# Optimization experiments

Measured on AMD Instinct MI355X. Metric: run time of the kernel, lower is better.

The kernel has to match this reference:

```python
import jax, jax.numpy as jnp
import numpy as np

NUM_NODES = 512

def chebyshev_convolution(laplacian, signal, weights, t0):
    # Faithful port of the torch helper, including tk_prev staying equal to
    # `laplacian` throughout the loop (as in the source).
    k = weights.shape[0]
    # t0 is the identity, so t0 @ signal == signal
    out = jnp.matmul(signal, weights[0])
    out = out + jnp.matmul(jnp.matmul(laplacian, signal), weights[1])
    tk_prev = laplacian
    tk = 2.0 * jnp.matmul(laplacian, laplacian) - t0
    for i in range(2, k):
        out = out + jnp.matmul(jnp.matmul(tk, signal), weights[i])
        tk = 2.0 * jnp.matmul(laplacian, tk) - tk_prev
    return out


def setup_inputs() -> dict:
    key = jax.random.key(0)
    ks = jax.random.split(key, 5)
    B, T, N, C_IN, C_OUT, CS, CD = 4, 12, NUM_NODES, 64, 64, 3, 6
    std_l = 0.1 / np.sqrt(N)
    std_t = 0.1 / np.sqrt(C_IN)
    x = jax.random.normal(ks[0], (B, T, N, C_IN), dtype=jnp.float32)
    ws = jax.random.uniform(ks[1], (N, N), jnp.float32, -std_l, std_l)
    ts = jax.random.uniform(ks[2], (CS, C_IN, C_OUT), jnp.float32, -std_t, std_t)
    wp = jax.random.uniform(ks[3], (C_IN, C_IN), jnp.float32, -std_t, std_t)
    td = jax.random.uniform(ks[4], (CD, C_IN, C_OUT), jnp.float32, -std_t, std_t)
    return {"x": x, "ws": ws, "ts": ts, "wp": wp, "td": td}


def reference(x, ws, ts, wp, td):
    N = NUM_NODES
    t0 = jnp.eye(N, dtype=x.dtype)
    # Static (SGC) branch: Chebyshev conv with learned static Laplacian ws
    out_s = chebyshev_convolution(ws, x, ts, t0)
    # Dynamic branch: data-dependent Laplacian wd = x @ (wp @ x^T)  -> (B,T,N,N)
    wd = jnp.matmul(x, jnp.matmul(wp, jnp.swapaxes(x, -2, -1)))
    wd = wd + jnp.min(wd)
    wd = wd / jnp.max(wd) / (N ** 2)
    out_d = chebyshev_convolution(wd, x, td, t0)
    return out_s + out_d
```

## Files before the change

kernel.cpp:

```cpp
#include <hip/hip_runtime.h>
#include <cstddef>
#include <cstdint>

#define NN 512
#define CC 64
#define BT 48

typedef __bf16 bf16_t;
typedef bf16_t bf16x8 __attribute__((ext_vector_type(8)));
typedef bf16_t bf16x4 __attribute__((ext_vector_type(4)));
typedef float f32x4 __attribute__((ext_vector_type(4)));

#define OFF_MN    0
#define OFF_MX    384
#define OFF_WSB   1024
#define OFF_WS2B  132096
#define OFF_XBT   263168
#define OFF_XNB   1049600
#define OFF_XNR   1836032
#define OFF_CS0   2622464
#define OFF_WEB   2647040
#define OFF_WER   2745344
#define OFF_VDY   2843648
#define OFF_T1T   2846720
#define OFF_T2T   2848768

__device__ __forceinline__ f32x4 mfma(bf16x8 a, bf16x8 b, f32x4 c) {
  return __builtin_amdgcn_mfma_f32_16x16x32_bf16(a, b, c, 0, 0, 0);
}
__device__ __forceinline__ int swz_chunk(int r, int c8) {
  return r * 64 + ((c8 ^ (r & 7)) << 3);
}
__device__ __forceinline__ int swz_e(int r, int c) {
  return r * 64 + ((((c >> 3) ^ (r & 7)) << 3)) + (c & 7);
}
__device__ __forceinline__ bf16x8 frag(const bf16_t* sm, int row, int kc) {
  return *(const bf16x8*)(sm + row * 64 + ((kc ^ (row & 7)) << 3));
}
__device__ __forceinline__ void stage64(bf16_t* sm, const bf16_t* g, int ld, int tid) {
#pragma unroll
  for (int j = 0; j < 2; ++j) {
    int id = tid + 256 * j;
    int r = id >> 3, c8 = id & 7;
    bf16x8 v = *(const bf16x8*)(g + (size_t)r * ld + c8 * 8);
    *(bf16x8*)(sm + swz_chunk(r, c8)) = v;
  }
}
__device__ __forceinline__ void stage64f(bf16_t* sm, const float* g, int ld, int tid) {
#pragma unroll
  for (int j = 0; j < 4; ++j) {
    int idx = tid + 256 * j;
    int r = idx >> 4, cc = (idx & 15) * 4;
    float4 v = *(const float4*)(g + (size_t)r * ld + cc);
    bf16x4 o = {(bf16_t)v.x, (bf16_t)v.y, (bf16_t)v.z, (bf16_t)v.w};
    *(bf16x4*)(sm + swz_e(r, cc)) = o;
  }
}
struct bfpair { bf16_t b, r; };
__device__ __forceinline__ bfpair splitbf(float f) {
  bfpair p;
  p.b = (bf16_t)f;
  p.r = (bf16_t)(f - (float)p.b);
  return p;
}

__global__ __launch_bounds__(256) void k_preA(
    const float* __restrict__ x, const float* __restrict__ wp,
    float* __restrict__ wsf)
{
  __shared__ __align__(16) char pool[32768];
  __shared__ float red[16];
  const int tid = threadIdx.x;
  const int b = blockIdx.x;
  const int w = tid >> 6, l = tid & 63, lh = l >> 4, lr = l & 15, m0 = w * 16;

  if (b < 384) {
    const int bt = (b & 7) + 8 * (b >> 6);
    const int it = (b >> 3) & 7;
    const int i0 = it * 64;
    float (*XsF)[66] = (float(*)[66])pool;
    bf16_t* XBT = (bf16_t*)(wsf + OFF_XBT);
    bf16_t* XNb = (bf16_t*)(wsf + OFF_XNB);
    bf16_t* XNr = (bf16_t*)(wsf + OFF_XNR);
    float* CS0 = wsf + OFF_CS0;
    const float* xg = x + ((size_t)bt * NN + i0) * CC;
    for (int j = 0; j < 4; ++j) {
      int idx = tid + 256 * j;
      int r = idx >> 4, c0v = (idx & 15) * 4;
      float4 v = *(const float4*)(xg + (size_t)r * CC + c0v);
      bfpair p0 = splitbf(v.x), p1 = splitbf(v.y), p2 = splitbf(v.z), p3 = splitbf(v.w);
      bf16x4 vb = {p0.b, p1.b, p2.b, p3.b};
      bf16x4 vr = {p0.r, p1.r, p2.r, p3.r};
      size_t gb = ((size_t)bt * 512 + i0 + r) * 64 + c0v;
      *(bf16x4*)(XNb + gb) = vb;
      *(bf16x4*)(XNr + gb) = vr;
      XsF[c0v + 0][r] = v.x; XsF[c0v + 1][r] = v.y;
      XsF[c0v + 2][r] = v.z; XsF[c0v + 3][r] = v.w;
    }
    __syncthreads();
    {
      int c = tid >> 2, k0 = (tid & 3) * 16;
      bf16x8 o1, o2;
#pragma unroll
      for (int q = 0; q < 8; ++q) {
        o1[q] = (bf16_t)XsF[c][k0 + q];
        o2[q] = (bf16_t)XsF[c][k0 + 8 + q];
      }
      size_t base = ((size_t)bt * 64 + c) * 512 + i0 + k0;
      *(bf16x8*)(XBT + base) = o1; *(bf16x8*)(XBT + base + 8) = o2;
    }
    if (tid < 64) {
      float s = 0.f;
      for (int r = 0; r < 64; ++r) s += XsF[tid][r];
      CS0[((size_t)bt * 8 + it) * 64 + tid] = s;
    }
    return;
  }
  const int g = b - 384;
  const int bt = (g & 7) + 8 * (g >> 6);
  const int bx = (g >> 3) & 7;
  bf16_t* WpT  = (bf16_t*)pool;
  bf16_t* Xa   = (bf16_t*)(pool + 8192);
  bf16_t* Hs   = (bf16_t*)(pool + 16384);
  bf16_t* Xcol = (bf16_t*)(pool + 24576);
  for (int j = 0; j < 4; ++j) {
    int idx = tid + 256 * j;
    int r = idx >> 4, cc = (idx & 15) * 4;
    float4 v = *(const float4*)(wp + r * 64 + cc);
    WpT[swz_e(cc + 0, r)] = (bf16_t)v.x;
    WpT[swz_e(cc + 1, r)] = (bf16_t)v.y;
    WpT[swz_e(cc + 2, r)] = (bf16_t)v.z;
    WpT[swz_e(cc + 3, r)] = (bf16_t)v.w;
  }
  stage64f(Xa, x + ((size_t)bt * NN + bx * 64) * CC, 64, tid);
  __syncthreads();
  f32x4 hacc[4] = {};
#pragma unroll
  for (int q = 0; q < 2; ++q) {
    bf16x8 a = frag(Xa, m0 + lr, q * 4 + lh);
#pragma unroll
    for (int t = 0; t < 4; ++t)
      hacc[t] = mfma(a, frag(WpT, t * 16 + lr, q * 4 + lh), hacc[t]);
  }
#pragma unroll
  for (int t = 0; t < 4; ++t)
#pragma unroll
    for (int r_ = 0; r_ < 4; ++r_)
      Hs[swz_e(m0 + 4 * lh + r_, t * 16 + lr)] = (bf16_t)hacc[t][r_];
  float mn = 3.4e38f, mx = -3.4e38f;
  for (int byj = 0; byj < 8; ++byj) {
    __syncthreads();
    stage64f(Xcol, x + ((size_t)bt * NN + byj * 64) * CC, 64, tid);
    __syncthreads();
    f32x4 acc[4] = {};
#pragma unroll
    for (int q = 0; q < 2; ++q) {
      bf16x8 a = frag(Hs, m0 + lr, q * 4 + lh);
#pragma unroll
      for (int t = 0; t < 4; ++t)
        acc[t] = mfma(a, frag(Xcol, t * 16 + lr, q * 4 + lh), acc[t]);
    }
#pragma unroll
    for (int t = 0; t < 4; ++t)
#pragma unroll
      for (int r_ = 0; r_ < 4; ++r_) {
        mn = fminf(mn, acc[t][r_]); mx = fmaxf(mx, acc[t][r_]);
      }
  }
  for (int off = 32; off; off >>= 1) {
    mn = fminf(mn, __shfl_xor(mn, off));
    mx = fmaxf(mx, __shfl_xor(mx, off));
  }
  if (l == 0) { red[w] = mn; red[8 + w] = mx; }
  __syncthreads();
  if (tid == 0) {
    mn = fminf(fminf(red[0], red[1]), fminf(red[2], red[3]));
    mx = fmaxf(fmaxf(red[8], red[9]), fmaxf(red[10], red[11]));
    wsf[OFF_MN + g] = mn; wsf[OFF_MX + g] = mx;
  }
}

__global__ __launch_bounds__(256) void k_mid(
    const float* __restrict__ wsL, const float* __restrict__ ts,
    const float* __restrict__ wp, const float* __restrict__ td,
    float* __restrict__ wsf)
{
  __shared__ __align__(16) char pool[91712];
  const int tid = threadIdx.x;
  const int b = blockIdx.x;
  const int w = tid >> 6, l = tid & 63, lh = l >> 4, lr = l & 15, m0 = w * 16;

  if (b >= 48) {
    if (b < 112) {
      const int idx2 = b - 48;
      bf16_t* Asb = (bf16_t*)pool;
      bf16_t* Bsb = (bf16_t*)(pool + 8192);
      bf16_t* Ys  = (bf16_t*)(pool + 16384);
      bf16_t* WS2B = (bf16_t*)(wsf + OFF_WS2B);
      const int r0 = (idx2 >> 3) * 64, c0 = (idx2 & 7) * 64;
      f32x4 acc[4] = {};
      for (int jj = 0; jj < 8; ++jj) {
        if (jj) __syncthreads();
        for (int j = 0; j < 4; ++j) {
          int idx = tid + 256 * j;
          int r = idx >> 4, cc = (idx & 15) * 4;
          float4 v = *(const float4*)(wsL + (size_t)(r0 + r) * 512 + jj * 64 + cc);
          bf16x4 vb = {(bf16_t)v.x, (bf16_t)v.y, (bf16_t)v.z, (bf16_t)v.w};
          *(bf16x4*)(Asb + swz_e(r, cc)) = vb;
          float4 u = *(const float4*)(wsL + (size_t)(jj * 64 + r) * 512 + c0 + cc);
          Bsb[swz_e(cc + 0, r)] = (bf16_t)u.x;
          Bsb[swz_e(cc + 1, r)] = (bf16_t)u.y;
          Bsb[swz_e(cc + 2, r)] = (bf16_t)u.z;
          Bsb[swz_e(cc + 3, r)] = (bf16_t)u.w;
        }
        __syncthreads();
#pragma unroll
        for (int q = 0; q < 2; ++q) {
          bf16x8 a = frag(Asb, m0 + lr, q * 4 + lh);
#pragma unroll
          for (int t = 0; t < 4; ++t)
            acc[t] = mfma(a, frag(Bsb, t * 16 + lr, q * 4 + lh), acc[t]);
        }
      }
#pragma unroll
      for (int t = 0; t < 4; ++t)
#pragma unroll
        for (int r_ = 0; r_ < 4; ++r_) {
          int row = m0 + 4 * lh + r_, col = t * 16 + lr;
          float v = 2.0f * acc[t][r_] - ((r0 + row) == (c0 + col) ? 1.0f : 0.0f);
          Ys[swz_e(row, col)] = (bf16_t)v;
        }
      __syncthreads();
#pragma unroll
      for (int j = 0; j < 2; ++j) {
        int id = tid + 256 * j;
        int r = id >> 3, c8 = id & 7;
        *(bf16x8*)(WS2B + (size_t)(r0 + r) * 512 + c0 + c8 * 8) =
            *(const bf16x8*)(Ys + swz_chunk(r, c8));
      }
      return;
    }
    if (b < 120) {
      const int bx = b - 112;
      const float* wrow = wsL + (size_t)bx * 64 * 512;
      bf16_t* wob = (bf16_t*)(wsf + OFF_WSB) + (size_t)bx * 64 * 512;
      for (int j = 0; j < 32; ++j) {
        int idx = tid + 256 * j;
        float4 v = *(const float4*)(wrow + (size_t)idx * 4);
        bf16x4 o = {(bf16_t)v.x, (bf16_t)v.y, (bf16_t)v.z, (bf16_t)v.w};
        *(bf16x4*)(wob + (size_t)idx * 4) = o;
      }
      return;
    }
    {
      bf16_t* T1 = (bf16_t*)(wsf + OFF_T1T);
      bf16_t* T2 = (bf16_t*)(wsf + OFF_T2T);
      const float* t1g = ts + 4096;
      const float* t2g = ts + 8192;
      for (int j = 0; j < 16; ++j) {
        int idx = tid + 256 * j;
        int cin = idx >> 6, co = idx & 63;
        T1[co * 64 + cin] = (bf16_t)t1g[cin * 64 + co];
        T2[co * 64 + cin] = (bf16_t)t2g[cin * 64 + co];
      }
      return;
    }
  }
  const int bt = b;
  bf16_t* XB  = (bf16_t*)pool;
  bf16_t* Ab0 = (bf16_t*)pool;
  bf16_t* AT0 = (bf16_t*)(pool + 8192);
  bf16_t* Ab1 = (bf16_t*)(pool + 16384);
  bf16_t* AT1 = (bf16_t*)(pool + 24576);
  bf16_t* Gb  = (bf16_t*)(pool + 32768);
  bf16_t* WpT = (bf16_t*)(pool + 40960);
  bf16_t* WpN = (bf16_t*)(pool + 49152);
  bf16_t* tdA = (bf16_t*)(pool + 57344);
  bf16_t* tdB = (bf16_t*)(pool + 65536);
  float (*P0F)[66] = (float(*)[66])(pool + 73728);
  float* vec = (float*)(pool + 90624);
  float* uF = vec;        float* hF = vec + 64;
  float* b0 = vec + 128;  float* b1 = vec + 192;
  float* redv = vec + 256;
  const bf16_t* XBTg = (const bf16_t*)(wsf + OFF_XBT);
  const float* CS0 = wsf + OFF_CS0;
  for (int kk = 0; kk < 8; ++kk)
    stage64(XB + kk * 4096, XBTg + (size_t)bt * 32768 + kk * 64, 512, tid);
  {
    float mn = 3.4e38f, mx = -3.4e38f;
    for (int i = tid; i < 384; i += 256) {
      mn = fminf(mn, wsf[OFF_MN + i]);
      mx = fmaxf(mx, wsf[OFF_MX + i]);
    }
    for (int off = 32; off; off >>= 1) {
      mn = fminf(mn, __shfl_xor(mn, off));
      mx = fmaxf(mx, __shfl_xor(mx, off));
    }
    if (l == 0) { redv[w] = mn; redv[8 + w] = mx; }
  }
  if (tid < 64) {
    float s = 0.f;
#pragma unroll
    for (int p = 0; p < 8; ++p) s += CS0[((size_t)bt * 8 + p) * 64 + tid];
    uF[tid] = s;
  }
  __syncthreads();
  f32x4 pacc[4] = {};
  for (int kk = 0; kk < 8; ++kk) {
    const bf16_t* xt = XB + kk * 4096;
#pragma unroll
    for (int q = 0; q < 2; ++q) {
      bf16x8 a = frag(xt, m0 + lr, q * 4 + lh);
#pragma unroll
      for (int t = 0; t < 4; ++t)
        pacc[t] = mfma(a, frag(xt, t * 16 + lr, q * 4 + lh), pacc[t]);
    }
  }
  const float mnA = fminf(fminf(redv[0], redv[1]), fminf(redv[2], redv[3]));
  const float mxA = fmaxf(fmaxf(redv[8], redv[9]), fmaxf(redv[10], redv[11]));
  const float s_sc = 1.0f / (mxA + mnA) / 262144.0f;
  const float c_sc = mnA * s_sc;
  __syncthreads();
#pragma unroll
  for (int t = 0; t < 4; ++t)
#pragma unroll
    for (int r_ = 0; r_ < 4; ++r_) {
      int m = m0 + 4 * lh + r_, jc = t * 16 + lr;
      float pv = pacc[t][r_];
      P0F[m][jc] = pv;
      bf16_t bv = (bf16_t)pv;
      Ab0[swz_e(m, jc)] = bv; AT0[swz_e(jc, m)] = bv;
    }
  for (int j = 0; j < 4; ++j) {
    int idx = tid + 256 * j;
    int r = idx >> 4, cc = (idx & 15) * 4;
    float4 v = *(const float4*)(wp + r * 64 + cc);
    bf16_t q0 = (bf16_t)v.x, q1 = (bf16_t)v.y, q2 = (bf16_t)v.z, q3 = (bf16_t)v.w;
    WpN[swz_e(r, cc + 0)] = q0; WpT[swz_e(cc + 0, r)] = q0;
    WpN[swz_e(r, cc + 1)] = q1; WpT[swz_e(cc + 1, r)] = q1;
    WpN[swz_e(r, cc + 2)] = q2; WpT[swz_e(cc + 2, r)] = q2;
    WpN[swz_e(r, cc + 3)] = q3; WpT[swz_e(cc + 3, r)] = q3;
  }
  for (int j = 0; j < 4; ++j) {
    int idx = tid + 256 * j;
    int cin = idx >> 4, co = (idx & 15) * 4;
    float4 v = *(const float4*)(td + 4096 + cin * 64 + co);
    tdA[swz_e(co + 0, cin)] = (bf16_t)v.x;
    tdA[swz_e(co + 1, cin)] = (bf16_t)v.y;
    tdA[swz_e(co + 2, cin)] = (bf16_t)v.z;
    tdA[swz_e(co + 3, cin)] = (bf16_t)v.w;
  }
  if (tid < 64) b0[tid] = uF[tid];
  __syncthreads();
  {
    int jj = tid >> 2, sub = tid & 3;
    float s = 0.f;
    for (int c = sub * 16; c < sub * 16 + 16; ++c)
      s += (float)WpT[swz_e(jj, c)] * uF[c];
    s += __shfl_xor(s, 1); s += __shfl_xor(s, 2);
    if (sub == 0) hF[jj] = s;
  }
  {
    f32x4 g[4] = {};
#pragma unroll
    for (int q = 0; q < 2; ++q) {
      bf16x8 a = frag(Ab0, m0 + lr, q * 4 + lh);
#pragma unroll
      for (int t = 0; t < 4; ++t)
        g[t] = mfma(a, frag(WpT, t * 16 + lr, q * 4 + lh), g[t]);
    }
#pragma unroll
    for (int t = 0; t < 4; ++t)
#pragma unroll
      for (int r_ = 0; r_ < 4; ++r_)
        Gb[swz_e(m0 + 4 * lh + r_, t * 16 + lr)] = (bf16_t)g[t][r_];
  }
  __syncthreads();
  float mu = 0.f, vacc = 0.f;
  f32x4 Macc[4] = {};
  for (int i = 1; i <= 5; ++i) {
    const float* bcur = (i & 1) ? b0 : b1;
    float* bnx = (i & 1) ? b1 : b0;
    const bf16_t* tdc = (i & 1) ? tdA : tdB;
    const bf16_t* AbC = (i & 1) ? Ab0 : Ab1;
    const bf16_t* ATC = (i & 1) ? AT0 : AT1;
    bf16_t* AbN = (i & 1) ? Ab1 : Ab0;
    bf16_t* ATN = (i & 1) ? AT1 : AT0;
    if (i < 5) {
      bf16_t* tdn = (i & 1) ? tdB : tdA;
      for (int j = 0; j < 4; ++j) {
        int idx = tid + 256 * j;
        int cin = idx >> 4, co = (idx & 15) * 4;
        float4 v = *(const float4*)(td + (i + 1) * 4096 + cin * 64 + co);
        tdn[swz_e(co + 0, cin)] = (bf16_t)v.x;
        tdn[swz_e(co + 1, cin)] = (bf16_t)v.y;
        tdn[swz_e(co + 2, cin)] = (bf16_t)v.z;
        tdn[swz_e(co + 3, cin)] = (bf16_t)v.w;
      }
    }
#pragma unroll
    for (int q = 0; q < 2; ++q) {
      bf16x8 a = frag(AbC, m0 + lr, q * 4 + lh);
#pragma unroll
      for (int t = 0; t < 4; ++t)
        Macc[t] = mfma(a, frag(tdc, t * 16 + lr, q * 4 + lh), Macc[t]);
    }
    f32x4 Aacc[4] = {};
    if (i < 5) {
#pragma unroll
      for (int q = 0; q < 2; ++q) {
        bf16x8 g = frag(Gb, m0 + lr, q * 4 + lh);
#pragma unroll
        for (int t = 0; t < 4; ++t)
          Aacc[t] = mfma(g, frag(ATC, t * 16 + lr, q * 4 + lh), Aacc[t]);
      }
    }
    {
      int co = tid >> 2, sub = tid & 3;
      float sv = 0.f;
      for (int c = sub * 16; c < sub * 16 + 16; ++c)
        sv += bcur[c] * (float)tdc[swz_e(co, c)];
      sv += __shfl_xor(sv, 1); sv += __shfl_xor(sv, 2);
      if (sub == 0) vacc += sv;
    }
    if (i < 5) {
      int jj = tid >> 2, sub = tid & 3;
      float t1 = 0.f;
      for (int m = sub * 16; m < sub * 16 + 16; ++m)
        t1 += (float)ATC[swz_e(jj, m)] * hF[m];
      t1 += __shfl_xor(t1, 1); t1 += __shfl_xor(t1, 2);
      if (sub == 0)
        bnx[jj] = 2.f * (s_sc * t1 + 512.f * c_sc * bcur[jj] + mu * uF[jj])
                  - (i >= 2 ? uF[jj] : 0.f);
    }
    if (i < 5) {
#pragma unroll
      for (int t = 0; t < 4; ++t)
#pragma unroll
        for (int r_ = 0; r_ < 4; ++r_) {
          int m = m0 + 4 * lh + r_, jc = t * 16 + lr;
          float v = 2.f * (s_sc * Aacc[t][r_] + c_sc * uF[m] * bcur[jc] + mu * P0F[m][jc])
                    - (i >= 2 ? P0F[m][jc] : 0.f);
          bf16_t bv = (bf16_t)v;
          AbN[swz_e(m, jc)] = bv; ATN[swz_e(jc, m)] = bv;
        }
      mu = (i == 1) ? -1.f : 0.f;
    }
    __syncthreads();
  }
  bf16_t* Mst = tdA;
#pragma unroll
  for (int t = 0; t < 4; ++t)
#pragma unroll
    for (int r_ = 0; r_ < 4; ++r_)
      Mst[swz_e(t * 16 + lr, m0 + 4 * lh + r_)] = (bf16_t)Macc[t][r_];
  __syncthreads();
  f32x4 wm[4] = {};
#pragma unroll
  for (int q = 0; q < 2; ++q) {
    bf16x8 a = frag(WpN, m0 + lr, q * 4 + lh);
#pragma unroll
    for (int t = 0; t < 4; ++t)
      wm[t] = mfma(a, frag(Mst, t * 16 + lr, q * 4 + lh), wm[t]);
  }
  bf16_t* WEb = (bf16_t*)(wsf + OFF_WEB);
  bf16_t* WEr = (bf16_t*)(wsf + OFF_WER);
#pragma unroll
  for (int t = 0; t < 4; ++t)
#pragma unroll
    for (int r_ = 0; r_ < 4; ++r_) {
      int a_ = m0 + 4 * lh + r_, co = t * 16 + lr;
      float weff = ts[a_ * 64 + co] + td[a_ * 64 + co] - td[2 * 4096 + a_ * 64 + co]
                   + s_sc * wm[t][r_];
      bfpair p = splitbf(weff);
      WEb[((size_t)bt * 64 + co) * 64 + a_] = p.b;
      WEr[((size_t)bt * 64 + co) * 64 + a_] = p.r;
    }
  if ((tid & 3) == 0) (wsf + OFF_VDY)[bt * 64 + (tid >> 2)] = c_sc * vacc;
}

__global__ __launch_bounds__(256) void k_out(float* __restrict__ wsf,
                                             float* __restrict__ out)
{
  __shared__ __align__(16) char pool[73728];
  bf16_t* As  = (bf16_t*)pool;
  bf16_t* B1  = (bf16_t*)(pool + 8192);
  bf16_t* B2  = (bf16_t*)(pool + 16384);
  bf16_t* Z1s = As;
  bf16_t* Z2s = B1;
  bf16_t* Xb  = (bf16_t*)(pool + 24576);
  bf16_t* Xr  = (bf16_t*)(pool + 32768);
  bf16_t* WEs = (bf16_t*)(pool + 40960);
  bf16_t* WRs = (bf16_t*)(pool + 49152);
  bf16_t* T1s = (bf16_t*)(pool + 57344);
  bf16_t* T2s = (bf16_t*)(pool + 65536);
  const int tid = threadIdx.x;
  const int g = blockIdx.x;
  const int bt = (g & 7) + 8 * (g >> 6);
  const int n0 = ((g >> 3) & 7) * 64;
  const int w = tid >> 6, l = tid & 63, lh = l >> 4, lr = l & 15, m0 = w * 16;
  stage64(Xb,  (const bf16_t*)(wsf + OFF_XNB) + ((size_t)bt * 512 + n0) * 64, 64, tid);
  stage64(Xr,  (const bf16_t*)(wsf + OFF_XNR) + ((size_t)bt * 512 + n0) * 64, 64, tid);
  stage64(WEs, (const bf16_t*)(wsf + OFF_WEB) + (size_t)bt * 4096, 64, tid);
  stage64(WRs, (const bf16_t*)(wsf + OFF_WER) + (size_t)bt * 4096, 64, tid);
  stage64(T1s, (const bf16_t*)(wsf + OFF_T1T), 64, tid);
  stage64(T2s, (const bf16_t*)(wsf + OFF_T2T), 64, tid);
  const bf16_t* XBT = (const bf16_t*)(wsf + OFF_XBT);
  const bf16_t* WSB = (const bf16_t*)(wsf + OFF_WSB);
  const bf16_t* WS2B = (const bf16_t*)(wsf + OFF_WS2B);
  f32x4 acc1[4] = {}, acc2[4] = {};
  for (int kk = 0; kk < 8; ++kk) {
    if (kk) __syncthreads();
    stage64(As, XBT + (size_t)bt * 32768 + kk * 64, 512, tid);
    stage64(B1, WSB + (size_t)n0 * 512 + kk * 64, 512, tid);
    stage64(B2, WS2B + (size_t)n0 * 512 + kk * 64, 512, tid);
    __syncthreads();
#pragma unroll
    for (int q = 0; q < 2; ++q) {
      bf16x8 a = frag(As, m0 + lr, q * 4 + lh);
#pragma unroll
      for (int t = 0; t < 4; ++t) {
        acc1[t] = mfma(a, frag(B1, t * 16 + lr, q * 4 + lh), acc1[t]);
        acc2[t] = mfma(a, frag(B2, t * 16 + lr, q * 4 + lh), acc2[t]);
      }
    }
  }
  __syncthreads();
#pragma unroll
  for (int t = 0; t < 4; ++t)
#pragma unroll
    for (int r_ = 0; r_ < 4; ++r_) {
      int cy = m0 + 4 * lh + r_, nl = t * 16 + lr;
      Z1s[swz_e(nl, cy)] = (bf16_t)acc1[t][r_];
      Z2s[swz_e(nl, cy)] = (bf16_t)acc2[t][r_];
    }
  __syncthreads();
  const float* VDY = wsf + OFF_VDY;
  f32x4 accO[4];
#pragma unroll
  for (int t = 0; t < 4; ++t) {
    float vv = VDY[bt * 64 + t * 16 + lr];
    accO[t] = {vv, vv, vv, vv};
  }
#pragma unroll
  for (int q = 0; q < 2; ++q) {
    bf16x8 aXb = frag(Xb, m0 + lr, q * 4 + lh);
    bf16x8 aXr = frag(Xr, m0 + lr, q * 4 + lh);
    bf16x8 aZ1 = frag(Z1s, m0 + lr, q * 4 + lh);
    bf16x8 aZ2 = frag(Z2s, m0 + lr, q * 4 + lh);
#pragma unroll
    for (int t = 0; t < 4; ++t) {
      bf16x8 bWb = frag(WEs, t * 16 + lr, q * 4 + lh);
      bf16x8 bWr = frag(WRs, t * 16 + lr, q * 4 + lh);
      accO[t] = mfma(aXb, bWb, accO[t]);
      accO[t] = mfma(aXb, bWr, accO[t]);
      accO[t] = mfma(aXr, bWb, accO[t]);
      accO[t] = mfma(aZ1, frag(T1s, t * 16 + lr, q * 4 + lh), accO[t]);
      accO[t] = mfma(aZ2, frag(T2s, t * 16 + lr, q * 4 + lh), accO[t]);
    }
  }
#pragma unroll
  for (int t = 0; t < 4; ++t)
#pragma unroll
    for (int r_ = 0; r_ < 4; ++r_)
      out[((size_t)bt * 512 + n0 + m0 + 4 * lh + r_) * 64 + t * 16 + lr] = accO[t][r_];
}

extern "C" void kernel_launch(void* const* d_in, const int* in_sizes, int n_in,
                              void* d_out, int out_size, void* d_ws, size_t ws_size,
                              hipStream_t stream)
{
  (void)in_sizes; (void)n_in; (void)out_size; (void)ws_size;
  const float* x   = (const float*)d_in[0];
  const float* wsL = (const float*)d_in[1];
  const float* ts  = (const float*)d_in[2];
  const float* wp  = (const float*)d_in[3];
  const float* td  = (const float*)d_in[4];
  float* out = (float*)d_out;
  float* wsf = (float*)d_ws;
  dim3 b(256);

  k_preA<<<768, b, 0, stream>>>(x, wp, wsf);
  k_mid <<<121, b, 0, stream>>>(wsL, ts, wp, td, wsf);
  k_out <<<384, b, 0, stream>>>(wsf, out);
}
```

Before: 44.66 us.

## Fuse per-batch weight derivation into output kernel, dropping the middle launch

The three-kernel pipeline becomes two. The static-Laplacian squaring, bf16 casting and transposes move into the prologue kernel. The per-bt Chebyshev recurrence that builds the effective weights now runs inside each output block, reusing the X^T X product it computes alongside the Z GEMMs. This removes a launch and the global round trip for WEb/WEr/VDY. In exchange, each bt's recurrence is repeated in 8 blocks, and the larger LDS footprint may lower occupancy.

```diff
diff --git a/kernel.cpp b/kernel.cpp
--- a/kernel.cpp
+++ b/kernel.cpp
@@ -19,11 +19,8 @@
 #define OFF_XNB   1049600
 #define OFF_XNR   1836032
 #define OFF_CS0   2622464
-#define OFF_WEB   2647040
-#define OFF_WER   2745344
-#define OFF_VDY   2843648
-#define OFF_T1T   2846720
-#define OFF_T2T   2848768
+#define OFF_T1T   2647040
+#define OFF_T2T   2649088
 
 __device__ __forceinline__ f32x4 mfma(bf16x8 a, bf16x8 b, f32x4 c) {
   return __builtin_amdgcn_mfma_f32_16x16x32_bf16(a, b, c, 0, 0, 0);
@@ -64,8 +61,9 @@
   return p;
 }
 
-__global__ __launch_bounds__(256) void k_preA(
-    const float* __restrict__ x, const float* __restrict__ wp,
+__global__ __launch_bounds__(256) void k_pre(
+    const float* __restrict__ x, const float* __restrict__ wsL,
+    const float* __restrict__ ts, const float* __restrict__ wp,
     float* __restrict__ wsf)
 {
   __shared__ __align__(16) char pool[32768];
@@ -116,158 +114,186 @@
     }
     return;
   }
-  const int g = b - 384;
+  if (b < 768) {
+    const int g = b - 384;
+    const int bt = (g & 7) + 8 * (g >> 6);
+    const int bx = (g >> 3) & 7;
+    bf16_t* WpT  = (bf16_t*)pool;
+    bf16_t* Xa   = (bf16_t*)(pool + 8192);
+    bf16_t* Hs   = (bf16_t*)(pool + 16384);
+    bf16_t* Xcol = (bf16_t*)(pool + 24576);
+    for (int j = 0; j < 4; ++j) {
+      int idx = tid + 256 * j;
+      int r = idx >> 4, cc = (idx & 15) * 4;
+      float4 v = *(const float4*)(wp + r * 64 + cc);
+      WpT[swz_e(cc + 0, r)] = (bf16_t)v.x;
+      WpT[swz_e(cc + 1, r)] = (bf16_t)v.y;
+      WpT[swz_e(cc + 2, r)] = (bf16_t)v.z;
+      WpT[swz_e(cc + 3, r)] = (bf16_t)v.w;
+    }
+    stage64f(Xa, x + ((size_t)bt * NN + bx * 64) * CC, 64, tid);
+    __syncthreads();
+    f32x4 hacc[4] = {};
+#pragma unroll
+    for (int q = 0; q < 2; ++q) {
+      bf16x8 a = frag(Xa, m0 + lr, q * 4 + lh);
+#pragma unroll
+      for (int t = 0; t < 4; ++t)
+        hacc[t] = mfma(a, frag(WpT, t * 16 + lr, q * 4 + lh), hacc[t]);
+    }
+#pragma unroll
+    for (int t = 0; t < 4; ++t)
+#pragma unroll
+      for (int r_ = 0; r_ < 4; ++r_)
+        Hs[swz_e(m0 + 4 * lh + r_, t * 16 + lr)] = (bf16_t)hacc[t][r_];
+    float mn = 3.4e38f, mx = -3.4e38f;
+    for (int byj = 0; byj < 8; ++byj) {
+      __syncthreads();
+      stage64f(Xcol, x + ((size_t)bt * NN + byj * 64) * CC, 64, tid);
+      __syncthreads();
+      f32x4 acc[4] = {};
+#pragma unroll
+      for (int q = 0; q < 2; ++q) {
+        bf16x8 a = frag(Hs, m0 + lr, q * 4 + lh);
+#pragma unroll
+        for (int t = 0; t < 4; ++t)
+          acc[t] = mfma(a, frag(Xcol, t * 16 + lr, q * 4 + lh), acc[t]);
+      }
+#pragma unroll
+      for (int t = 0; t < 4; ++t)
+#pragma unroll
+        for (int r_ = 0; r_ < 4; ++r_) {
+          mn = fminf(mn, acc[t][r_]); mx = fmaxf(mx, acc[t][r_]);
+        }
+    }
+    for (int off = 32; off; off >>= 1) {
+      mn = fminf(mn, __shfl_xor(mn, off));
+      mx = fmaxf(mx, __shfl_xor(mx, off));
+    }
+    if (l == 0) { red[w] = mn; red[8 + w] = mx; }
+    __syncthreads();
+    if (tid == 0) {
+      mn = fminf(fminf(red[0], red[1]), fminf(red[2], red[3]));
+      mx = fmaxf(fmaxf(red[8], red[9]), fmaxf(red[10], red[11]));
+      wsf[OFF_MN + g] = mn; wsf[OFF_MX + g] = mx;
+    }
+    return;
+  }
+  if (b < 832) {
+    const int idx2 = b - 768;
+    bf16_t* Asb = (bf16_t*)pool;
+    bf16_t* Bsb = (bf16_t*)(pool + 8192);
+    bf16_t* Ys  = (bf16_t*)(pool + 16384);
+    bf16_t* WS2B = (bf16_t*)(wsf + OFF_WS2B);
+    const int r0 = (idx2 >> 3) * 64, c0 = (idx2 & 7) * 64;
+    f32x4 acc[4] = {};
+    for (int jj = 0; jj < 8; ++jj) {
+      if (jj) __syncthreads();
+      for (int j = 0; j < 4; ++j) {
+        int idx = tid + 256 * j;
+        int r = idx >> 4, cc = (idx & 15) * 4;
+        float4 v = *(const float4*)(wsL + (size_t)(r0 + r) * 512 + jj * 64 + cc);
+        bf16x4 vb = {(bf16_t)v.x, (bf16_t)v.y, (bf16_t)v.z, (bf16_t)v.w};
+        *(bf16x4*)(Asb + swz_e(r, cc)) = vb;
+        float4 u = *(const float4*)(wsL + (size_t)(jj * 64 + r) * 512 + c0 + cc);
+        Bsb[swz_e(cc + 0, r)] = (bf16_t)u.x;
+        Bsb[swz_e(cc + 1, r)] = (bf16_t)u.y;
+        Bsb[swz_e(cc + 2, r)] = (bf16_t)u.z;
+        Bsb[swz_e(cc + 3, r)] = (bf16_t)u.w;
+      }
+      __syncthreads();
+#pragma unroll
+      for (int q = 0; q < 2; ++q) {
+        bf16x8 a = frag(Asb, m0 + lr, q * 4 + lh);
+#pragma unroll
+        for (int t = 0; t < 4; ++t)
+          acc[t] = mfma(a, frag(Bsb, t * 16 + lr, q * 4 + lh), acc[t]);
+      }
+    }
+#pragma unroll
+    for (int t = 0; t < 4; ++t)
+#pragma unroll
+      for (int r_ = 0; r_ < 4; ++r_) {
+        int row = m0 + 4 * lh + r_, col = t * 16 + lr;
+        float v = 2.0f * acc[t][r_] - ((r0 + row) == (c0 + col) ? 1.0f : 0.0f);
+        Ys[swz_e(row, col)] = (bf16_t)v;
+      }
+    __syncthreads();
+#pragma unroll
+    for (int j = 0; j < 2; ++j) {
+      int id = tid + 256 * j;
+      int r = id >> 3, c8 = id & 7;
+      *(bf16x8*)(WS2B + (size_t)(r0 + r) * 512 + c0 + c8 * 8) =
+          *(const bf16x8*)(Ys + swz_chunk(r, c8));
+    }
+    return;
+  }
+  if (b < 840) {
+    const int bx = b - 832;
+    const float* wrow = wsL + (size_t)bx * 64 * 512;
+    bf16_t* wob = (bf16_t*)(wsf + OFF_WSB) + (size_t)bx * 64 * 512;
+    for (int j = 0; j < 32; ++j) {
+      int idx = tid + 256 * j;
+      float4 v = *(const float4*)(wrow + (size_t)idx * 4);
+      bf16x4 o = {(bf16_t)v.x, (bf16_t)v.y, (bf16_t)v.z, (bf16_t)v.w};
+      *(bf16x4*)(wob + (size_t)idx * 4) = o;
+    }
+    return;
+  }
+  {
+    bf16_t* T1 = (bf16_t*)(wsf + OFF_T1T);
+    bf16_t* T2 = (bf16_t*)(wsf + OFF_T2T);
+    const float* t1g = ts + 4096;
+    const float* t2g = ts + 8192;
+    for (int j = 0; j < 16; ++j) {
+      int idx = tid + 256 * j;
+      int cin = idx >> 6, co = idx & 63;
+      T1[co * 64 + cin] = (bf16_t)t1g[cin * 64 + co];
+      T2[co * 64 + cin] = (bf16_t)t2g[cin * 64 + co];
+    }
+  }
+}
+
+__global__ __launch_bounds__(256) void k_go(
+    const float* __restrict__ ts, const float* __restrict__ wp,
+    const float* __restrict__ td, float* __restrict__ wsf,
+    float* __restrict__ out)
+{
+  __shared__ __align__(16) char pool[81920];
+  const int tid = threadIdx.x;
+  const int g = blockIdx.x;
   const int bt = (g & 7) + 8 * (g >> 6);
-  const int bx = (g >> 3) & 7;
-  bf16_t* WpT  = (bf16_t*)pool;
-  bf16_t* Xa   = (bf16_t*)(pool + 8192);
-  bf16_t* Hs   = (bf16_t*)(pool + 16384);
-  bf16_t* Xcol = (bf16_t*)(pool + 24576);
-  for (int j = 0; j < 4; ++j) {
-    int idx = tid + 256 * j;
-    int r = idx >> 4, cc = (idx & 15) * 4;
-    float4 v = *(const float4*)(wp + r * 64 + cc);
-    WpT[swz_e(cc + 0, r)] = (bf16_t)v.x;
-    WpT[swz_e(cc + 1, r)] = (bf16_t)v.y;
-    WpT[swz_e(cc + 2, r)] = (bf16_t)v.z;
-    WpT[swz_e(cc + 3, r)] = (bf16_t)v.w;
-  }
-  stage64f(Xa, x + ((size_t)bt * NN + bx * 64) * CC, 64, tid);
+  const int n0 = ((g >> 3) & 7) * 64;
+  const int w = tid >> 6, l = tid & 63, lh = l >> 4, lr = l & 15, m0 = w * 16;
+
+  bf16_t* XB = (bf16_t*)pool;
+  bf16_t* B1 = (bf16_t*)(pool + 65536);
+  bf16_t* B2 = (bf16_t*)(pool + 73728);
+  const bf16_t* XBTg = (const bf16_t*)(wsf + OFF_XBT);
+  const bf16_t* WSB  = (const bf16_t*)(wsf + OFF_WSB);
+  const bf16_t* WS2B = (const bf16_t*)(wsf + OFF_WS2B);
+  for (int kk = 0; kk < 8; ++kk)
+    stage64(XB + kk * 4096, XBTg + (size_t)bt * 32768 + kk * 64, 512, tid);
+  f32x4 acc1[4] = {}, acc2[4] = {}, pacc[4] = {};
+  for (int kk = 0; kk < 8; ++kk) {
+    __syncthreads();
+    stage64(B1, WSB + (size_t)n0 * 512 + kk * 64, 512, tid);
+    stage64(B2, WS2B + (size_t)n0 * 512 + kk * 64, 512, tid);
+    __syncthreads();
+    const bf16_t* xt = XB + kk * 4096;
+#pragma unroll
+    for (int q = 0; q < 2; ++q) {
+      bf16x8 a = frag(xt, m0 + lr, q * 4 + lh);
+#pragma unroll
+      for (int t = 0; t < 4; ++t) {
+        acc1[t] = mfma(a, frag(B1, t * 16 + lr, q * 4 + lh), acc1[t]);
+        acc2[t] = mfma(a, frag(B2, t * 16 + lr, q * 4 + lh), acc2[t]);
+        pacc[t] = mfma(a, frag(xt, t * 16 + lr, q * 4 + lh), pacc[t]);
+      }
+    }
+  }
   __syncthreads();
-  f32x4 hacc[4] = {};
-#pragma unroll
-  for (int q = 0; q < 2; ++q) {
-    bf16x8 a = frag(Xa, m0 + lr, q * 4 + lh);
-#pragma unroll
-    for (int t = 0; t < 4; ++t)
-      hacc[t] = mfma(a, frag(WpT, t * 16 + lr, q * 4 + lh), hacc[t]);
-  }
-#pragma unroll
-  for (int t = 0; t < 4; ++t)
-#pragma unroll
-    for (int r_ = 0; r_ < 4; ++r_)
-      Hs[swz_e(m0 + 4 * lh + r_, t * 16 + lr)] = (bf16_t)hacc[t][r_];
-  float mn = 3.4e38f, mx = -3.4e38f;
-  for (int byj = 0; byj < 8; ++byj) {
-    __syncthreads();
-    stage64f(Xcol, x + ((size_t)bt * NN + byj * 64) * CC, 64, tid);
-    __syncthreads();
-    f32x4 acc[4] = {};
-#pragma unroll
-    for (int q = 0; q < 2; ++q) {
-      bf16x8 a = frag(Hs, m0 + lr, q * 4 + lh);
-#pragma unroll
-      for (int t = 0; t < 4; ++t)
-        acc[t] = mfma(a, frag(Xcol, t * 16 + lr, q * 4 + lh), acc[t]);
-    }
-#pragma unroll
-    for (int t = 0; t < 4; ++t)
-#pragma unroll
-      for (int r_ = 0; r_ < 4; ++r_) {
-        mn = fminf(mn, acc[t][r_]); mx = fmaxf(mx, acc[t][r_]);
-      }
-  }
-  for (int off = 32; off; off >>= 1) {
-    mn = fminf(mn, __shfl_xor(mn, off));
-    mx = fmaxf(mx, __shfl_xor(mx, off));
-  }
-  if (l == 0) { red[w] = mn; red[8 + w] = mx; }
-  __syncthreads();
-  if (tid == 0) {
-    mn = fminf(fminf(red[0], red[1]), fminf(red[2], red[3]));
-    mx = fmaxf(fmaxf(red[8], red[9]), fmaxf(red[10], red[11]));
-    wsf[OFF_MN + g] = mn; wsf[OFF_MX + g] = mx;
-  }
-}
-
-__global__ __launch_bounds__(256) void k_mid(
-    const float* __restrict__ wsL, const float* __restrict__ ts,
-    const float* __restrict__ wp, const float* __restrict__ td,
-    float* __restrict__ wsf)
-{
-  __shared__ __align__(16) char pool[91712];
-  const int tid = threadIdx.x;
-  const int b = blockIdx.x;
-  const int w = tid >> 6, l = tid & 63, lh = l >> 4, lr = l & 15, m0 = w * 16;
-
-  if (b >= 48) {
-    if (b < 112) {
-      const int idx2 = b - 48;
-      bf16_t* Asb = (bf16_t*)pool;
-      bf16_t* Bsb = (bf16_t*)(pool + 8192);
-      bf16_t* Ys  = (bf16_t*)(pool + 16384);
-      bf16_t* WS2B = (bf16_t*)(wsf + OFF_WS2B);
-      const int r0 = (idx2 >> 3) * 64, c0 = (idx2 & 7) * 64;
-      f32x4 acc[4] = {};
-      for (int jj = 0; jj < 8; ++jj) {
-        if (jj) __syncthreads();
-        for (int j = 0; j < 4; ++j) {
-          int idx = tid + 256 * j;
-          int r = idx >> 4, cc = (idx & 15) * 4;
-          float4 v = *(const float4*)(wsL + (size_t)(r0 + r) * 512 + jj * 64 + cc);
-          bf16x4 vb = {(bf16_t)v.x, (bf16_t)v.y, (bf16_t)v.z, (bf16_t)v.w};
-          *(bf16x4*)(Asb + swz_e(r, cc)) = vb;
-          float4 u = *(const float4*)(wsL + (size_t)(jj * 64 + r) * 512 + c0 + cc);
-          Bsb[swz_e(cc + 0, r)] = (bf16_t)u.x;
-          Bsb[swz_e(cc + 1, r)] = (bf16_t)u.y;
-          Bsb[swz_e(cc + 2, r)] = (bf16_t)u.z;
-          Bsb[swz_e(cc + 3, r)] = (bf16_t)u.w;
-        }
-        __syncthreads();
-#pragma unroll
-        for (int q = 0; q < 2; ++q) {
-          bf16x8 a = frag(Asb, m0 + lr, q * 4 + lh);
-#pragma unroll
-          for (int t = 0; t < 4; ++t)
-            acc[t] = mfma(a, frag(Bsb, t * 16 + lr, q * 4 + lh), acc[t]);
-        }
-      }
-#pragma unroll
-      for (int t = 0; t < 4; ++t)
-#pragma unroll
-        for (int r_ = 0; r_ < 4; ++r_) {
-          int row = m0 + 4 * lh + r_, col = t * 16 + lr;
-          float v = 2.0f * acc[t][r_] - ((r0 + row) == (c0 + col) ? 1.0f : 0.0f);
-          Ys[swz_e(row, col)] = (bf16_t)v;
-        }
-      __syncthreads();
-#pragma unroll
-      for (int j = 0; j < 2; ++j) {
-        int id = tid + 256 * j;
-        int r = id >> 3, c8 = id & 7;
-        *(bf16x8*)(WS2B + (size_t)(r0 + r) * 512 + c0 + c8 * 8) =
-            *(const bf16x8*)(Ys + swz_chunk(r, c8));
-      }
-      return;
-    }
-    if (b < 120) {
-      const int bx = b - 112;
-      const float* wrow = wsL + (size_t)bx * 64 * 512;
-      bf16_t* wob = (bf16_t*)(wsf + OFF_WSB) + (size_t)bx * 64 * 512;
-      for (int j = 0; j < 32; ++j) {
-        int idx = tid + 256 * j;
-        float4 v = *(const float4*)(wrow + (size_t)idx * 4);
-        bf16x4 o = {(bf16_t)v.x, (bf16_t)v.y, (bf16_t)v.z, (bf16_t)v.w};
-        *(bf16x4*)(wob + (size_t)idx * 4) = o;
-      }
-      return;
-    }
-    {
-      bf16_t* T1 = (bf16_t*)(wsf + OFF_T1T);
-      bf16_t* T2 = (bf16_t*)(wsf + OFF_T2T);
-      const float* t1g = ts + 4096;
-      const float* t2g = ts + 8192;
-      for (int j = 0; j < 16; ++j) {
-        int idx = tid + 256 * j;
-        int cin = idx >> 6, co = idx & 63;
-        T1[co * 64 + cin] = (bf16_t)t1g[cin * 64 + co];
-        T2[co * 64 + cin] = (bf16_t)t2g[cin * 64 + co];
-      }
-      return;
-    }
-  }
-  const int bt = b;
-  bf16_t* XB  = (bf16_t*)pool;
+
   bf16_t* Ab0 = (bf16_t*)pool;
   bf16_t* AT0 = (bf16_t*)(pool + 8192);
   bf16_t* Ab1 = (bf16_t*)(pool + 16384);
@@ -277,15 +303,12 @@
   bf16_t* WpN = (bf16_t*)(pool + 49152);
   bf16_t* tdA = (bf16_t*)(pool + 57344);
   bf16_t* tdB = (bf16_t*)(pool + 65536);
-  float (*P0F)[66] = (float(*)[66])(pool + 73728);
-  float* vec = (float*)(pool + 90624);
-  float* uF = vec;        float* hF = vec + 64;
-  float* b0 = vec + 128;  float* b1 = vec + 192;
-  float* redv = vec + 256;
-  const bf16_t* XBTg = (const bf16_t*)(wsf + OFF_XBT);
+  float* vec = (float*)(pool + 73728);
+  float* uF = vec;         float* hF = vec + 64;
+  float* b0 = vec + 128;   float* b1 = vec + 192;
+  float* vaccF = vec + 256;
+  float* redv = vec + 320;
   const float* CS0 = wsf + OFF_CS0;
-  for (int kk = 0; kk < 8; ++kk)
-    stage64(XB + kk * 4096, XBTg + (size_t)bt * 32768 + kk * 64, 512, tid);
   {
     float mn = 3.4e38f, mx = -3.4e38f;
     for (int i = tid; i < 384; i += 256) {
@@ -298,39 +321,20 @@
     }
     if (l == 0) { redv[w] = mn; redv[8 + w] = mx; }
   }
+#pragma unroll
+  for (int t = 0; t < 4; ++t)
+#pragma unroll
+    for (int r_ = 0; r_ < 4; ++r_) {
+      int m = m0 + 4 * lh + r_, jc = t * 16 + lr;
+      bf16_t bv = (bf16_t)pacc[t][r_];
+      Ab0[swz_e(m, jc)] = bv; AT0[swz_e(jc, m)] = bv;
+    }
   if (tid < 64) {
     float s = 0.f;
 #pragma unroll
     for (int p = 0; p < 8; ++p) s += CS0[((size_t)bt * 8 + p) * 64 + tid];
-    uF[tid] = s;
-  }
-  __syncthreads();
-  f32x4 pacc[4] = {};
-  for (int kk = 0; kk < 8; ++kk) {
-    const bf16_t* xt = XB + kk * 4096;
-#pragma unroll
-    for (int q = 0; q < 2; ++q) {
-      bf16x8 a = frag(xt, m0 + lr, q * 4 + lh);
-#pragma unroll
-      for (int t = 0; t < 4; ++t)
-        pacc[t] = mfma(a, frag(xt, t * 16 + lr, q * 4 + lh), pacc[t]);
-    }
-  }
-  const float mnA = fminf(fminf(redv[0], redv[1]), fminf(redv[2], redv[3]));
-  const float mxA = fmaxf(fmaxf(redv[8], redv[9]), fmaxf(redv[10], redv[11]));
-  const float s_sc = 1.0f / (mxA + mnA) / 262144.0f;
-  const float c_sc = mnA * s_sc;
-  __syncthreads();
-#pragma unroll
-  for (int t = 0; t < 4; ++t)
-#pragma unroll
-    for (int r_ = 0; r_ < 4; ++r_) {
-      int m = m0 + 4 * lh + r_, jc = t * 16 + lr;
-      float pv = pacc[t][r_];
-      P0F[m][jc] = pv;
-      bf16_t bv = (bf16_t)pv;
-      Ab0[swz_e(m, jc)] = bv; AT0[swz_e(jc, m)] = bv;
-    }
+    uF[tid] = s; b0[tid] = s; vaccF[tid] = 0.f;
+  }
   for (int j = 0; j < 4; ++j) {
     int idx = tid + 256 * j;
     int r = idx >> 4, cc = (idx & 15) * 4;
@@ -350,8 +354,11 @@
     tdA[swz_e(co + 2, cin)] = (bf16_t)v.z;
     tdA[swz_e(co + 3, cin)] = (bf16_t)v.w;
   }
-  if (tid < 64) b0[tid] = uF[tid];
   __syncthreads();
+  const float mnA = fminf(fminf(redv[0], redv[1]), fminf(redv[2], redv[3]));
+  const float mxA = fmaxf(fmaxf(redv[8], redv[9]), fmaxf(redv[10], redv[11]));
+  const float s_sc = 1.0f / (mxA + mnA) / 262144.0f;
+  const float c_sc = mnA * s_sc;
   {
     int jj = tid >> 2, sub = tid & 3;
     float s = 0.f;
@@ -361,22 +368,22 @@
     if (sub == 0) hF[jj] = s;
   }
   {
-    f32x4 g[4] = {};
+    f32x4 gv[4] = {};
 #pragma unroll
     for (int q = 0; q < 2; ++q) {
       bf16x8 a = frag(Ab0, m0 + lr, q * 4 + lh);
 #pragma unroll
       for (int t = 0; t < 4; ++t)
-        g[t] = mfma(a, frag(WpT, t * 16 + lr, q * 4 + lh), g[t]);
+        gv[t] = mfma(a, frag(WpT, t * 16 + lr, q * 4 + lh), gv[t]);
     }
 #pragma unroll
     for (int t = 0; t < 4; ++t)
 #pragma unroll
       for (int r_ = 0; r_ < 4; ++r_)
-        Gb[swz_e(m0 + 4 * lh + r_, t * 16 + lr)] = (bf16_t)g[t][r_];
+        Gb[swz_e(m0 + 4 * lh + r_, t * 16 + lr)] = (bf16_t)gv[t][r_];
   }
   __syncthreads();
-  float mu = 0.f, vacc = 0.f;
+  float mu = 0.f;
   f32x4 Macc[4] = {};
   for (int i = 1; i <= 5; ++i) {
     const float* bcur = (i & 1) ? b0 : b1;
@@ -409,10 +416,10 @@
     if (i < 5) {
 #pragma unroll
       for (int q = 0; q < 2; ++q) {
-        bf16x8 g = frag(Gb, m0 + lr, q * 4 + lh);
+        bf16x8 gfr = frag(Gb, m0 + lr, q * 4 + lh);
 #pragma unroll
         for (int t = 0; t < 4; ++t)
-          Aacc[t] = mfma(g, frag(ATC, t * 16 + lr, q * 4 + lh), Aacc[t]);
+          Aacc[t] = mfma(gfr, frag(ATC, t * 16 + lr, q * 4 + lh), Aacc[t]);
       }
     }
     {
@@ -421,7 +428,7 @@
       for (int c = sub * 16; c < sub * 16 + 16; ++c)
         sv += bcur[c] * (float)tdc[swz_e(co, c)];
       sv += __shfl_xor(sv, 1); sv += __shfl_xor(sv, 2);
-      if (sub == 0) vacc += sv;
+      if (sub == 0) vaccF[co] += sv;
     }
     if (i < 5) {
       int jj = tid >> 2, sub = tid & 3;
@@ -439,8 +446,8 @@
 #pragma unroll
         for (int r_ = 0; r_ < 4; ++r_) {
           int m = m0 + 4 * lh + r_, jc = t * 16 + lr;
-          float v = 2.f * (s_sc * Aacc[t][r_] + c_sc * uF[m] * bcur[jc] + mu * P0F[m][jc])
-                    - (i >= 2 ? P0F[m][jc] : 0.f);
+          float v = 2.f * (s_sc * Aacc[t][r_] + c_sc * uF[m] * bcur[jc] + mu * pacc[t][r_])
+                    - (i >= 2 ? pacc[t][r_] : 0.f);
           bf16_t bv = (bf16_t)v;
           AbN[swz_e(m, jc)] = bv; ATN[swz_e(jc, m)] = bv;
         }
@@ -463,8 +470,16 @@
     for (int t = 0; t < 4; ++t)
       wm[t] = mfma(a, frag(Mst, t * 16 + lr, q * 4 + lh), wm[t]);
   }
-  bf16_t* WEb = (bf16_t*)(wsf + OFF_WEB);
-  bf16_t* WEr = (bf16_t*)(wsf + OFF_WER);
+  __syncthreads();
+
+  bf16_t* Z1s = (bf16_t*)pool;
+  bf16_t* Z2s = (bf16_t*)(pool + 8192);
+  bf16_t* Xb  = (bf16_t*)(pool + 16384);
+  bf16_t* Xr  = (bf16_t*)(pool + 24576);
+  bf16_t* WEs = (bf16_t*)(pool + 32768);
+  bf16_t* WRs = (bf16_t*)(pool + 40960);
+  bf16_t* T1s = (bf16_t*)(pool + 49152);
+  bf16_t* T2s = (bf16_t*)(pool + 57344);
 #pragma unroll
   for (int t = 0; t < 4; ++t)
 #pragma unroll
@@ -473,73 +488,21 @@
       float weff = ts[a_ * 64 + co] + td[a_ * 64 + co] - td[2 * 4096 + a_ * 64 + co]
                    + s_sc * wm[t][r_];
       bfpair p = splitbf(weff);
-      WEb[((size_t)bt * 64 + co) * 64 + a_] = p.b;
-      WEr[((size_t)bt * 64 + co) * 64 + a_] = p.r;
-    }
-  if ((tid & 3) == 0) (wsf + OFF_VDY)[bt * 64 + (tid >> 2)] = c_sc * vacc;
-}
-
-__global__ __launch_bounds__(256) void k_out(float* __restrict__ wsf,
-                                             float* __restrict__ out)
-{
-  __shared__ __align__(16) char pool[73728];
-  bf16_t* As  = (bf16_t*)pool;
-  bf16_t* B1  = (bf16_t*)(pool + 8192);
-  bf16_t* B2  = (bf16_t*)(pool + 16384);
-  bf16_t* Z1s = As;
-  bf16_t* Z2s = B1;
-  bf16_t* Xb  = (bf16_t*)(pool + 24576);
-  bf16_t* Xr  = (bf16_t*)(pool + 32768);
-  bf16_t* WEs = (bf16_t*)(pool + 40960);
-  bf16_t* WRs = (bf16_t*)(pool + 49152);
-  bf16_t* T1s = (bf16_t*)(pool + 57344);
-  bf16_t* T2s = (bf16_t*)(pool + 65536);
-  const int tid = threadIdx.x;
-  const int g = blockIdx.x;
-  const int bt = (g & 7) + 8 * (g >> 6);
-  const int n0 = ((g >> 3) & 7) * 64;
-  const int w = tid >> 6, l = tid & 63, lh = l >> 4, lr = l & 15, m0 = w * 16;
+      WEs[swz_e(co, a_)] = p.b;
+      WRs[swz_e(co, a_)] = p.r;
+      int cy = a_, nl = co;
+      Z1s[swz_e(nl, cy)] = (bf16_t)acc1[t][r_];
+      Z2s[swz_e(nl, cy)] = (bf16_t)acc2[t][r_];
+    }
   stage64(Xb,  (const bf16_t*)(wsf + OFF_XNB) + ((size_t)bt * 512 + n0) * 64, 64, tid);
   stage64(Xr,  (const bf16_t*)(wsf + OFF_XNR) + ((size_t)bt * 512 + n0) * 64, 64, tid);
-  stage64(WEs, (const bf16_t*)(wsf + OFF_WEB) + (size_t)bt * 4096, 64, tid);
-  stage64(WRs, (const bf16_t*)(wsf + OFF_WER) + (size_t)bt * 4096, 64, tid);
   stage64(T1s, (const bf16_t*)(wsf + OFF_T1T), 64, tid);
   stage64(T2s, (const bf16_t*)(wsf + OFF_T2T), 64, tid);
-  const bf16_t* XBT = (const bf16_t*)(wsf + OFF_XBT);
-  const bf16_t* WSB = (const bf16_t*)(wsf + OFF_WSB);
-  const bf16_t* WS2B = (const bf16_t*)(wsf + OFF_WS2B);
-  f32x4 acc1[4] = {}, acc2[4] = {};
-  for (int kk = 0; kk < 8; ++kk) {
-    if (kk) __syncthreads();
-    stage64(As, XBT + (size_t)bt * 32768 + kk * 64, 512, tid);
-    stage64(B1, WSB + (size_t)n0 * 512 + kk * 64, 512, tid);
-    stage64(B2, WS2B + (size_t)n0 * 512 + kk * 64, 512, tid);
-    __syncthreads();
-#pragma unroll
-    for (int q = 0; q < 2; ++q) {
-      bf16x8 a = frag(As, m0 + lr, q * 4 + lh);
-#pragma unroll
-      for (int t = 0; t < 4; ++t) {
-        acc1[t] = mfma(a, frag(B1, t * 16 + lr, q * 4 + lh), acc1[t]);
-        acc2[t] = mfma(a, frag(B2, t * 16 + lr, q * 4 + lh), acc2[t]);
-      }
-    }
-  }
   __syncthreads();
-#pragma unroll
-  for (int t = 0; t < 4; ++t)
-#pragma unroll
-    for (int r_ = 0; r_ < 4; ++r_) {
-      int cy = m0 + 4 * lh + r_, nl = t * 16 + lr;
-      Z1s[swz_e(nl, cy)] = (bf16_t)acc1[t][r_];
-      Z2s[swz_e(nl, cy)] = (bf16_t)acc2[t][r_];
-    }
-  __syncthreads();
-  const float* VDY = wsf + OFF_VDY;
   f32x4 accO[4];
 #pragma unroll
   for (int t = 0; t < 4; ++t) {
-    float vv = VDY[bt * 64 + t * 16 + lr];
+    float vv = c_sc * vaccF[t * 16 + lr];
     accO[t] = {vv, vv, vv, vv};
   }
 #pragma unroll
@@ -580,7 +543,6 @@
   float* wsf = (float*)d_ws;
   dim3 b(256);
 
-  k_preA<<<768, b, 0, stream>>>(x, wp, wsf);
-  k_mid <<<121, b, 0, stream>>>(wsL, ts, wp, td, wsf);
-  k_out <<<384, b, 0, stream>>>(wsf, out);
-}
+  k_pre<<<841, b, 0, stream>>>(x, wsL, ts, wp, wsf);
+  k_go <<<384, b, 0, stream>>>(ts, wp, td, wsf, out);
+}
```

New measurement: 48.34 us. +8.2%, slower.
